# Kernel optimization log

Hardware: AMD Instinct MI355X
Metric: run time of the kernel (lower is better)

## Reference

```python
import jax, jax.numpy as jnp
import numpy as np

PAD = 0
EPS = 1e-5


def setup_inputs() -> dict:
    key = jax.random.key(0)
    k1, k2, k3, k4, k5 = jax.random.split(key, 5)
    B, S, D, H = 16, 1024, 512, 4
    output = jax.random.normal(k1, (B, S, D), dtype=jnp.float32)
    local_cor = jax.random.normal(k2, (1,), dtype=jnp.float32)
    event_type = jax.random.randint(k3, (B, S), 0, 1000, dtype=jnp.int64)
    # xavier-ish scale for the per-layer Linear weights
    W = jax.random.normal(k4, (H, D, D), dtype=jnp.float32) * (1.0 / np.sqrt(D))
    b = jax.random.normal(k5, (H, D), dtype=jnp.float32) * 0.01
    return {"output": output, "local_cor": local_cor, "event_type": event_type, "W": W, "b": b}


def _build_mask(event_type, S, dtype):
    # subsequent mask: 1 for strictly-future positions (triu, diag=1)
    subseq = jnp.triu(jnp.ones((S, S), dtype=dtype), k=1)  # [S,S]
    # key-pad mask: 1 where key token is PAD, broadcast over query dim
    keypad = (event_type == PAD).astype(dtype)[:, None, :]  # [B,1,S]
    return ((keypad + subseq[None]) > 0).astype(dtype)  # [B,S,S]


def reference(output, local_cor, event_type, W, b):
    B, S, D = output.shape
    H = W.shape[0]
    temperature = jnp.asarray(D, output.dtype) ** 0.5
    mask = _build_mask(event_type, S, output.dtype)  # [B,S,S]

    x = output
    total = None
    for h in range(H):  # heads are applied SEQUENTIALLY in the original
        # masked QK^T scores
        attn = jnp.einsum('bqd,bkd->bqk', x / temperature, x) * mask  # [B,S,S]
        # L2 normalize along keys (F.normalize p=2, eps=1e-5)
        norm = jnp.sqrt(jnp.sum(attn * attn, axis=-1, keepdims=True))
        attn = attn / jnp.maximum(norm, EPS)
        # value path: ELU(Linear(x))
        v = jax.nn.elu(jnp.einsum('bsd,ed->bse', x, W[h]) + b[h])  # [B,S,D]
        x = jnp.einsum('bqk,bkd->bqd', attn, v)
        total = x if total is None else total + x
    return total
```

## Files before the change

kernel.cpp:

```cpp
#include <hip/hip_runtime.h>
#include <math.h>

#define B_ 16
#define S_ 1024
#define D_ 512
#define H_ 4
#define INV_TEMP 0.044194173824159216f
#define C_SCALE 0.00390625f
#define OUT_SCALE 256.0f

typedef _Float16 f16;
typedef _Float16 f16x8 __attribute__((ext_vector_type(8)));
typedef _Float16 f16x4 __attribute__((ext_vector_type(4)));
typedef float f32x4 __attribute__((ext_vector_type(4)));

#define AS1(p) ((const __attribute__((address_space(1))) void*)(p))
#define AS3(p) ((__attribute__((address_space(3))) void*)(p))
#define MFMA __builtin_amdgcn_mfma_f32_16x16x32_f16

__global__ __launch_bounds__(256)
void k_conv(const float* __restrict__ src, f16* __restrict__ dst)
{
    const int i = blockIdx.x * 256 + threadIdx.x;
    const float4 v = ((const float4*)src)[i];
    f16x4 h; h[0] = (f16)v.x; h[1] = (f16)v.y; h[2] = (f16)v.z; h[3] = (f16)v.w;
    ((f16x4*)dst)[i] = h;
}

__global__ __launch_bounds__(128)
void k_flags(const int* __restrict__ etype, int* __restrict__ flag)
{
    const int t = threadIdx.x;
    const int b = t >> 3, kt = t & 7;
    const int* p = etype + b * S_ + kt * 128;
    int any0 = 0;
#pragma unroll
    for (int i = 0; i < 128; i += 4) {
        const int4 v = *(const int4*)(p + i);
        any0 |= (v.x == 0) | (v.y == 0) | (v.z == 0) | (v.w == 0);
    }
    flag[t] = any0;
}

__device__ __forceinline__ void stage128x32(const f16* __restrict__ src, int ld,
                                            char* lds0, int t)
{
    const f16* g0 = src + (size_t)(t >> 2) * ld + (t & 3) * 8;
    __builtin_amdgcn_global_load_lds(AS1(g0), AS3(lds0 + t * 16), 16, 0, 0);
    const f16* g1 = g0 + (size_t)64 * ld;
    __builtin_amdgcn_global_load_lds(AS1(g1), AS3(lds0 + 4096 + t * 16), 16, 0, 0);
}

__device__ __forceinline__ void mma_chunk(const char* ldsA, const char* ldsB,
                                          int wm, int wn, int lr, int quad,
                                          f32x4 (*acc)[4])
{
    f16x8 af[4], bf[4];
#pragma unroll
    for (int i = 0; i < 4; ++i)
        af[i] = *(const f16x8*)(ldsA + ((wm * 64 + i * 16 + lr) * 32 + quad * 8) * 2);
#pragma unroll
    for (int j = 0; j < 4; ++j)
        bf[j] = *(const f16x8*)(ldsB + ((wn * 64 + j * 16 + lr) * 32 + quad * 8) * 2);
#pragma unroll
    for (int i = 0; i < 4; ++i)
#pragma unroll
        for (int j = 0; j < 4; ++j)
            acc[i][j] = MFMA(af[i], bf[j], acc[i][j], 0, 0, 0);
}

__device__ __forceinline__ void gemm_core(const f16* A, int ldA, const f16* Bm, int ldB,
                                          int K, char* lds, int t, int wm, int wn,
                                          int lr, int quad, f32x4 (*acc)[4])
{
    for (int k0 = 0; k0 < K; k0 += 32) {
        stage128x32(A + k0, ldA, lds, t);
        stage128x32(Bm + k0, ldB, lds + 8192, t);
        __syncthreads();
        mma_chunk(lds, lds + 8192, wm, wn, lr, quad, acc);
        __syncthreads();
    }
}

__global__ __launch_bounds__(256)
void k_vs(const f16* __restrict__ xh, const f16* __restrict__ Wh,
          const float* __restrict__ bias, f16* __restrict__ vT,
          const int* __restrict__ etype, const int* __restrict__ flag,
          f16* __restrict__ sh, float* __restrict__ ss)
{
    __shared__ __align__(16) char lds[16384];
    const int t = threadIdx.x;
    const int w = t >> 6, lane = t & 63, lr = lane & 15, quad = lane >> 4;
    const int wm = w & 1, wn = w >> 1;

    if (blockIdx.x < 1024) {
        const int i0 = blockIdx.x;
        const int xcd = i0 & 7, j0 = i0 >> 3;
        const int b = 2 * xcd + (j0 & 1);
        const int tile = j0 >> 1;
        const int bk = (tile & 7) * 128;
        const int bq = (tile >> 3) * 128;
        if (bk < bq && !flag[b * 8 + (bk >> 7)]) return;

        const f16* xb = xh + (size_t)b * S_ * D_;
        f32x4 acc[4][4] = {};
        gemm_core(xb + (size_t)bk * D_, D_, xb + (size_t)bq * D_, D_, D_,
                  lds, t, wm, wn, lr, quad, acc);
        const float sc = INV_TEMP * C_SCALE;
        float ssq[4] = {0.0f, 0.0f, 0.0f, 0.0f};
#pragma unroll
        for (int i = 0; i < 4; ++i) {
            const int k4 = bk + wm * 64 + i * 16 + quad * 4;
            const int4 et = *(const int4*)(etype + b * S_ + k4);
            const int ev[4] = {et.x, et.y, et.z, et.w};
#pragma unroll
            for (int j = 0; j < 4; ++j) {
                const int q = bq + wn * 64 + j * 16 + lr;
                f16x4 hv;
#pragma unroll
                for (int r = 0; r < 4; ++r) {
                    const bool keep = ((k4 + r) > q) || (ev[r] == 0);
                    hv[r] = (f16)(keep ? acc[i][j][r] * sc : 0.0f);
                    const float fv = (float)hv[r];
                    ssq[j] += fv * fv;
                }
                *(f16x4*)(sh + ((size_t)b * S_ + q) * S_ + k4) = hv;
            }
        }
#pragma unroll
        for (int j = 0; j < 4; ++j) {
            float v = ssq[j];
            v += __shfl_xor(v, 16, 64);
            v += __shfl_xor(v, 32, 64);
            if (quad == 0) {
                const int q = bq + wn * 64 + j * 16 + lr;
                atomicAdd(ss + b * S_ + q, v);
            }
        }
    } else {
        const int idx = blockIdx.x - 1024;
        const int bm = (idx & 127) * 128;
        const int bn = (idx >> 7) * 128;
        f32x4 acc[4][4] = {};
        gemm_core(xh + (size_t)bm * D_, D_, Wh + (size_t)bn * D_, D_, D_,
                  lds, t, wm, wn, lr, quad, acc);
#pragma unroll
        for (int j = 0; j < 4; ++j) {
            const int e = bn + wn * 64 + j * 16 + lr;
            const float be = bias[e];
#pragma unroll
            for (int i = 0; i < 4; ++i) {
                const int m = bm + wm * 64 + i * 16 + quad * 4;
                const int batch = m >> 10, s = m & 1023;
                f16x4 hv;
#pragma unroll
                for (int r = 0; r < 4; ++r) {
                    float z = acc[i][j][r] + be;
                    z = (z > 0.0f) ? z : (expf(z) - 1.0f);
                    hv[r] = (f16)z;
                }
                *(f16x4*)(vT + ((size_t)batch * D_ + e) * S_ + s) = hv;
            }
        }
    }
}

__global__ __launch_bounds__(512)
void k_out(const f16* __restrict__ vT, const f16* __restrict__ sh,
           const float* __restrict__ ss, const int* __restrict__ flag,
           f16* __restrict__ xh_w,
           const f16* __restrict__ xs0, const f16* __restrict__ xs1,
           const f16* __restrict__ xs2,
           float* __restrict__ out, const int accum, const int wout)
{
    __shared__ __align__(16) char lds[65536];
    __shared__ int klist[32];
    __shared__ int kcnt;
    const int t = threadIdx.x;
    const int g = t >> 8;
    const int tl = t & 255;
    const int w = tl >> 6, lane = tl & 63, lr = lane & 15, quad = lane >> 4;
    const int wm = w & 1, wn = w >> 1;
    const int i0 = blockIdx.x;
    const int xcd = i0 & 7, j0 = i0 >> 3;
    const int b = 2 * xcd + (j0 & 1);
    const int tile = j0 >> 1;
    const int be = (tile & 3) * 128;
    const int bq = (tile >> 2) * 128;
    const int qt = bq >> 7;

    if (t == 0) {
        int n = 0;
        for (int kc = 0; kc < 8; ++kc)
            if (kc >= qt || flag[b * 8 + kc]) {
                const int kb = kc * 128;
                klist[n] = kb; klist[n + 1] = kb + 32;
                klist[n + 2] = kb + 64; klist[n + 3] = kb + 96;
                n += 4;
            }
        kcnt = n;
    }
    __syncthreads();
    const int half = kcnt >> 1;
    const int s0 = g ? half : 0;

    const f16* Abase = vT + ((size_t)b * D_ + be) * S_;
    const f16* Bbase = sh + ((size_t)b * S_ + bq) * S_;
    char* myl = lds + (g << 14);
    f32x4 acc[4][4] = {};
#pragma unroll 1
    for (int i = 0; i < half; ++i) {
        const int k0 = klist[s0 + i];
        stage128x32(Abase + k0, S_, myl, tl);
        stage128x32(Bbase + k0, S_, myl + 8192, tl);
        __syncthreads();
        mma_chunk(myl, myl + 8192, wm, wn, lr, quad, acc);
        __syncthreads();
    }

    if (g == 1) {
#pragma unroll
        for (int j = 0; j < 4; ++j)
#pragma unroll
            for (int i = 0; i < 4; ++i)
                *(f32x4*)(lds + (((w * 16 + j * 4 + i) * 64 + lane) << 4)) = acc[i][j];
    }
    __syncthreads();
    if (g == 0) {
#pragma unroll
        for (int j = 0; j < 4; ++j) {
            const int q = bq + wn * 64 + j * 16 + lr;
            const float ssv = ss[b * S_ + q];
            const float scl = 1.0f / (C_SCALE * fmaxf(sqrtf(ssv) * OUT_SCALE, 1e-5f));
#pragma unroll
            for (int i = 0; i < 4; ++i) {
                const f32x4 other =
                    *(const f32x4*)(lds + (((w * 16 + j * 4 + i) * 64 + lane) << 4));
                const f32x4 sum = acc[i][j] + other;
                const int e4 = be + wm * 64 + i * 16 + quad * 4;
                const size_t o = ((size_t)b * S_ + q) * D_ + e4;
                f32x4 val;
                f16x4 hx;
#pragma unroll
                for (int r = 0; r < 4; ++r) {
                    val[r] = sum[r] * scl;
                    hx[r] = (f16)val[r];
                }
                if (xh_w) *(f16x4*)(xh_w + o) = hx;
                if (xs0) {
                    const f16x4 a0 = *(const f16x4*)(xs0 + o);
                    const f16x4 a1 = *(const f16x4*)(xs1 + o);
                    const f16x4 a2 = *(const f16x4*)(xs2 + o);
#pragma unroll
                    for (int r = 0; r < 4; ++r)
                        val[r] += (float)a0[r] + (float)a1[r] + (float)a2[r];
                }
                if (wout) {
                    f32x4 v2 = val;
                    if (accum) { const f32x4 old = *(const f32x4*)(out + o); v2 = v2 + old; }
                    *(f32x4*)(out + o) = v2;
                }
            }
        }
    }
}

extern "C" void kernel_launch(void* const* d_in, const int* in_sizes, int n_in,
                              void* d_out, int out_size, void* d_ws, size_t ws_size,
                              hipStream_t stream) {
    const float* x0    = (const float*)d_in[0];
    const int*   etype = (const int*)d_in[2];
    const float* W     = (const float*)d_in[3];
    const float* bias  = (const float*)d_in[4];
    float* out = (float*)d_out;

    char* ws = (char*)d_ws;
    f16*   xA    = (f16*)(ws);
    f16*   vT    = (f16*)(ws + (16u << 20));
    f16*   sh    = (f16*)(ws + (32u << 20));
    f16*   Wh    = (f16*)(ws + (64u << 20));
    float* ssb   = (float*)(ws + (66u << 20));
    int*   flags = (int*)(ws + (66u << 20) + 262144);

    const bool big = ws_size >= ((size_t)101 << 20);
    f16* xB = big ? (f16*)(ws + (68u << 20)) : xA;
    f16* xC = big ? (f16*)(ws + (84u << 20)) : xA;

    k_conv <<<8192, 256, 0, stream>>>(x0, xA);
    k_conv <<<1024, 256, 0, stream>>>(W, Wh);
    k_flags<<<1, 128, 0, stream>>>(etype, flags);
    hipMemsetAsync(ssb, 0, 4 * (size_t)B_ * S_ * sizeof(float), stream);

    f16* xin[H_]  = {xA, xA, xB, xC};
    f16* xdst[H_] = {xA, xB, xC, nullptr};

    for (int h = 0; h < H_; ++h) {
        float* ss = ssb + (size_t)h * B_ * S_;
        k_vs <<<1536, 256, 0, stream>>>(xin[h], Wh + (size_t)h * D_ * D_,
                                        bias + (size_t)h * D_, vT,
                                        etype, flags, sh, ss);
        if (big) {
            const bool last = (h == H_ - 1);
            k_out<<<512, 512, 0, stream>>>(vT, sh, ss, flags, xdst[h],
                                           last ? xA : nullptr,
                                           last ? xB : nullptr,
                                           last ? xC : nullptr,
                                           out, 0, last ? 1 : 0);
        } else {
            k_out<<<512, 512, 0, stream>>>(vT, sh, ss, flags,
                                           (h < H_ - 1) ? xA : nullptr,
                                           nullptr, nullptr, nullptr,
                                           out, h > 0, 1);
        }
    }
}
```

Before: 363.4 us.

## Double K-step to 64 with XOR-swizzled LDS and shared diagonal tile

The staging and MFMA helpers now work on 128x64 K-chunks instead of 128x32, which halves the number of barrier pairs per GEMM. LDS rows are XOR-swizzled by row to avoid bank conflicts on the wider rows. On diagonal score tiles (bk == bq), only one operand is loaded and used as both A and B. LDS use grows to 32 KB per group, which may reduce occupancy.

```diff
diff --git a/kernel.cpp b/kernel.cpp
--- a/kernel.cpp
+++ b/kernel.cpp
@@ -42,42 +42,57 @@
     flag[t] = any0;
 }
 
-__device__ __forceinline__ void stage128x32(const f16* __restrict__ src, int ld,
+__device__ __forceinline__ void stage128x64(const f16* __restrict__ src, int ld,
                                             char* lds0, int t)
 {
-    const f16* g0 = src + (size_t)(t >> 2) * ld + (t & 3) * 8;
-    __builtin_amdgcn_global_load_lds(AS1(g0), AS3(lds0 + t * 16), 16, 0, 0);
-    const f16* g1 = g0 + (size_t)64 * ld;
-    __builtin_amdgcn_global_load_lds(AS1(g1), AS3(lds0 + 4096 + t * 16), 16, 0, 0);
-}
-
-__device__ __forceinline__ void mma_chunk(const char* ldsA, const char* ldsB,
-                                          int wm, int wn, int lr, int quad,
-                                          f32x4 (*acc)[4])
-{
-    f16x8 af[4], bf[4];
-#pragma unroll
-    for (int i = 0; i < 4; ++i)
-        af[i] = *(const f16x8*)(ldsA + ((wm * 64 + i * 16 + lr) * 32 + quad * 8) * 2);
+    const int r = t >> 3;
+    const int c = ((t & 7) ^ (r & 7)) << 3;
+    const f16* g = src + (size_t)r * ld + c;
 #pragma unroll
     for (int j = 0; j < 4; ++j)
-        bf[j] = *(const f16x8*)(ldsB + ((wn * 64 + j * 16 + lr) * 32 + quad * 8) * 2);
-#pragma unroll
-    for (int i = 0; i < 4; ++i)
-#pragma unroll
-        for (int j = 0; j < 4; ++j)
-            acc[i][j] = MFMA(af[i], bf[j], acc[i][j], 0, 0, 0);
-}
-
-__device__ __forceinline__ void gemm_core(const f16* A, int ldA, const f16* Bm, int ldB,
-                                          int K, char* lds, int t, int wm, int wn,
-                                          int lr, int quad, f32x4 (*acc)[4])
-{
-    for (int k0 = 0; k0 < K; k0 += 32) {
-        stage128x32(A + k0, ldA, lds, t);
-        stage128x32(Bm + k0, ldB, lds + 8192, t);
+        __builtin_amdgcn_global_load_lds(AS1(g + (size_t)(32 * j) * ld),
+                                         AS3(lds0 + j * 4096 + t * 16), 16, 0, 0);
+}
+
+__device__ __forceinline__ void mma64(const char* ldsA, const char* ldsB,
+                                      int wm, int wn, int lr, int quad,
+                                      f32x4 (*acc)[4])
+{
+#pragma unroll
+    for (int kk = 0; kk < 2; ++kk) {
+        f16x8 af[4], bf[4];
+#pragma unroll
+        for (int i = 0; i < 4; ++i) {
+            const int row = wm * 64 + i * 16 + lr;
+            af[i] = *(const f16x8*)(ldsA + (row << 7) +
+                                    ((((kk << 2) + quad) ^ (row & 7)) << 4));
+        }
+#pragma unroll
+        for (int j = 0; j < 4; ++j) {
+            const int row = wn * 64 + j * 16 + lr;
+            bf[j] = *(const f16x8*)(ldsB + (row << 7) +
+                                    ((((kk << 2) + quad) ^ (row & 7)) << 4));
+        }
+#pragma unroll
+        for (int i = 0; i < 4; ++i)
+#pragma unroll
+            for (int j = 0; j < 4; ++j)
+                acc[i][j] = MFMA(af[i], bf[j], acc[i][j], 0, 0, 0);
+    }
+}
+
+__device__ __forceinline__ void gemm_core64(const f16* A, int ldA,
+                                            const f16* Bm, int ldB,
+                                            int K, char* lds, int t,
+                                            int wm, int wn, int lr, int quad,
+                                            f32x4 (*acc)[4], bool diag)
+{
+    char* lb = diag ? lds : lds + 16384;
+    for (int k0 = 0; k0 < K; k0 += 64) {
+        stage128x64(A + k0, ldA, lds, t);
+        if (!diag) stage128x64(Bm + k0, ldB, lb, t);
         __syncthreads();
-        mma_chunk(lds, lds + 8192, wm, wn, lr, quad, acc);
+        mma64(lds, lb, wm, wn, lr, quad, acc);
         __syncthreads();
     }
 }
@@ -88,7 +103,7 @@
           const int* __restrict__ etype, const int* __restrict__ flag,
           f16* __restrict__ sh, float* __restrict__ ss)
 {
-    __shared__ __align__(16) char lds[16384];
+    __shared__ __align__(16) char lds[32768];
     const int t = threadIdx.x;
     const int w = t >> 6, lane = t & 63, lr = lane & 15, quad = lane >> 4;
     const int wm = w & 1, wn = w >> 1;
@@ -104,8 +119,8 @@
 
         const f16* xb = xh + (size_t)b * S_ * D_;
         f32x4 acc[4][4] = {};
-        gemm_core(xb + (size_t)bk * D_, D_, xb + (size_t)bq * D_, D_, D_,
-                  lds, t, wm, wn, lr, quad, acc);
+        gemm_core64(xb + (size_t)bk * D_, D_, xb + (size_t)bq * D_, D_, D_,
+                    lds, t, wm, wn, lr, quad, acc, bk == bq);
         const float sc = INV_TEMP * C_SCALE;
         float ssq[4] = {0.0f, 0.0f, 0.0f, 0.0f};
 #pragma unroll
@@ -142,8 +157,8 @@
         const int bm = (idx & 127) * 128;
         const int bn = (idx >> 7) * 128;
         f32x4 acc[4][4] = {};
-        gemm_core(xh + (size_t)bm * D_, D_, Wh + (size_t)bn * D_, D_, D_,
-                  lds, t, wm, wn, lr, quad, acc);
+        gemm_core64(xh + (size_t)bm * D_, D_, Wh + (size_t)bn * D_, D_, D_,
+                    lds, t, wm, wn, lr, quad, acc, false);
 #pragma unroll
         for (int j = 0; j < 4; ++j) {
             const int e = bn + wn * 64 + j * 16 + lr;
@@ -206,15 +221,15 @@
 
     const f16* Abase = vT + ((size_t)b * D_ + be) * S_;
     const f16* Bbase = sh + ((size_t)b * S_ + bq) * S_;
-    char* myl = lds + (g << 14);
+    char* myl = lds + (g << 15);
     f32x4 acc[4][4] = {};
 #pragma unroll 1
-    for (int i = 0; i < half; ++i) {
+    for (int i = 0; i < half; i += 2) {
         const int k0 = klist[s0 + i];
-        stage128x32(Abase + k0, S_, myl, tl);
-        stage128x32(Bbase + k0, S_, myl + 8192, tl);
+        stage128x64(Abase + k0, S_, myl, tl);
+        stage128x64(Bbase + k0, S_, myl + 16384, tl);
         __syncthreads();
-        mma_chunk(myl, myl + 8192, wm, wn, lr, quad, acc);
+        mma64(myl, myl + 16384, wm, wn, lr, quad, acc);
         __syncthreads();
     }
 
```

After: 350.4 us. 3.6% less time.
